# Performance work log

Measured on AMD Instinct MI355X. Metric: run time of the kernel, lower is better.

## Reference

```python
import jax, jax.numpy as jnp
import numpy as np

NUM_CLASSES = 19
TEMPERATURE = 0.2


def setup_inputs() -> dict:
    key = jax.random.key(0)
    k1, k2, k3 = jax.random.split(key, 3)
    fea = jax.random.normal(k1, (8, 256, 128, 128), dtype=jnp.float32)
    res = jax.random.normal(k2, (8, 19, 128, 128), dtype=jnp.float32)
    q = jax.random.normal(k3, (NUM_CLASSES, 256, 2975), dtype=jnp.float32)
    # buffers are L2-normalized along the feature (inner_planes) dim at init
    queues = q / jnp.maximum(jnp.linalg.norm(q, axis=1, keepdims=True), 1e-12)
    return {"fea": fea, "res": res, "queues": queues}


def _contrast_loss(fea, res, queues):
    # fea: [bs, C, H, W], res: [bs, K, H, W] logits, queues: [K, C, Q]
    bs, C = fea.shape[0], fea.shape[1]
    pred = jnp.argmax(res, axis=1).reshape(bs, -1)          # [bs, HW]
    ff = fea.reshape(bs, C, -1)                              # [bs, C, HW]

    # masked per-class region pooling across the whole batch (pred == val)
    onehot = (pred[:, :, None] == jnp.arange(NUM_CLASSES)[None, None, :]).astype(fea.dtype)  # [bs, HW, K]
    counts = onehot.sum(axis=(0, 1))                         # [K]
    sums = jnp.einsum('bcp,bpk->kc', ff, onehot)             # [K, C]
    keys = sums / jnp.maximum(counts, 1.0)[:, None]          # masked mean per class
    # F.normalize(keys, dim=1) with eps=1e-12
    keys = keys / jnp.maximum(jnp.linalg.norm(keys, axis=1, keepdims=True), 1e-12)

    # l_pos = q[:,None] * queue_c ; l_neg = q[:,None] * sum_{c'!=c} queue_c'
    qsum = queues.sum(axis=0)                                # [C, Q]
    l_pos = keys[:, :, None] * queues                        # [K, C, Q]
    l_neg = keys[:, :, None] * (qsum[None] - queues)         # [K, C, Q]
    logits = jnp.concatenate([l_pos, l_neg], axis=2) / TEMPERATURE  # [K, C, 2Q]

    # CrossEntropyLoss with labels all zero: mean over rows of (logsumexp - logit_0)
    lse = jax.nn.logsumexp(logits, axis=2)                   # [K, C]
    per_class = jnp.mean(lse - logits[:, :, 0], axis=1)      # [K]

    # original sums loss only over classes present in pred
    present = counts > 0
    return jnp.sum(jnp.where(present, per_class, jnp.zeros_like(per_class)))


def reference(fea, res, queues):
    contrast_loss = _contrast_loss(fea, res, queues)
    return (res, contrast_loss)
```

## Files before the change

kernel.cpp:

```cpp
#include <hip/hip_runtime.h>

#define HW 16384
#define BS 8
#define NC 256
#define K  19
#define Q  2975
#define INV_T 5.0f
#define NCHUNK 4
#define QC 744
#define NB1 512

__global__ void __launch_bounds__(256) k1_argmax(const float* __restrict__ res,
                                                 float* __restrict__ out,
                                                 unsigned char* __restrict__ pred,
                                                 int* __restrict__ histb,
                                                 float* __restrict__ sums) {
    __shared__ int hist[K];
    int t = threadIdx.x;
    if (t < K) hist[t] = 0;
    __syncthreads();
    int gp = blockIdx.x * 256 + t;
    int b  = gp >> 14;
    int p  = gp & (HW - 1);
    const float* rb = res + (size_t)b * K * HW + p;
    float*       ob = out + (size_t)b * K * HW + p;
    float best = rb[0];
    int   bk   = 0;
    __builtin_nontemporal_store(best, &ob[0]);
    #pragma unroll
    for (int k = 1; k < K; ++k) {
        float v = rb[(size_t)k * HW];
        __builtin_nontemporal_store(v, &ob[(size_t)k * HW]);
        if (v > best) { best = v; bk = k; }
    }
    pred[gp] = (unsigned char)bk;
    atomicAdd(&hist[bk], 1);
    if (blockIdx.x == 0) {
        for (int i = t; i < K * NC; i += 256) sums[i] = 0.f;
    }
    __syncthreads();
    if (t < K) histb[t * NB1 + blockIdx.x] = hist[t];
}

__global__ void __launch_bounds__(256) k2_pool(const float* __restrict__ fea,
                                               const unsigned char* __restrict__ pred,
                                               float* __restrict__ sums) {
    __shared__ float acc[K * 256];
    int t = threadIdx.x, lane = t & 63, w = t >> 6;
    int b = blockIdx.x >> 8;
    int c = blockIdx.x & 255;
    #pragma unroll
    for (int k = 0; k < K; ++k) acc[k * 256 + t] = 0.f;
    __syncthreads();
    const float4* f4 = (const float4*)(fea + (size_t)(b * NC + c) * HW);
    const uchar4* p4 = (const uchar4*)(pred + (size_t)b * HW);
    int c0 = t, c1 = (t + 64) & 255, c2 = (t + 128) & 255, c3 = (t + 192) & 255;
    #pragma unroll 2
    for (int i = t; i < HW / 4; i += 256) {
        float4 v  = f4[i];
        uchar4 kk = p4[i];
        int i0 = kk.x * 256 + c0, i1 = kk.y * 256 + c1;
        int i2 = kk.z * 256 + c2, i3 = kk.w * 256 + c3;
        float a0 = acc[i0], a1 = acc[i1], a2 = acc[i2], a3 = acc[i3];
        acc[i0] = a0 + v.x;
        acc[i1] = a1 + v.y;
        acc[i2] = a2 + v.z;
        acc[i3] = a3 + v.w;
    }
    __syncthreads();
    for (int k = w; k < K; k += 4) {
        float v = acc[k * 256 + lane]       + acc[k * 256 + lane + 64]
                + acc[k * 256 + lane + 128] + acc[k * 256 + lane + 192];
        #pragma unroll
        for (int off = 32; off > 0; off >>= 1) v += __shfl_xor(v, off, 64);
        if (lane == 0) atomicAdd(&sums[k * NC + c], v);
    }
}

__global__ void __launch_bounds__(256, 4) k4_lse(const float* __restrict__ queues,
                                                 const float* __restrict__ sums,
                                                 float* __restrict__ spart,
                                                 float* __restrict__ pos0) {
    int t = threadIdx.x;
    int c = blockIdx.x;
    int chunk = blockIdx.y;
    int lane = t & 63, wv = t >> 6;

    __shared__ float sc_sh[K];
    for (int k = wv; k < K; k += 4) {
        float ss = 0.f;
        #pragma unroll
        for (int j = 0; j < 4; ++j) {
            float v = sums[k * NC + j * 64 + lane];
            ss += v * v;
        }
        #pragma unroll
        for (int off = 32; off > 0; off >>= 1) ss += __shfl_xor(ss, off, 64);
        if (lane == 0) sc_sh[k] = INV_T / fmaxf(sqrtf(ss), 1e-12f);
    }
    __syncthreads();

    float key[K], s[K];
    #pragma unroll
    for (int k = 0; k < K; ++k) {
        key[k] = sums[k * NC + c] * sc_sh[k];
        s[k] = 0.f;
    }
    if (chunk == 0 && t < K)
        pos0[t * NC + c] = sums[t * NC + c] * sc_sh[t] * queues[(size_t)(t * NC + c) * Q];

    int q0 = chunk * QC;
    int qhi = min(Q, q0 + QC);
    for (int q = q0 + t; q < qhi; q += 256) {
        float qv[K];
        float qs = 0.f;
        #pragma unroll
        for (int k = 0; k < K; ++k) {
            qv[k] = queues[(size_t)(k * NC + c) * Q + q];
            qs += qv[k];
        }
        #pragma unroll
        for (int k = 0; k < K; ++k) {
            float a  = key[k] * qv[k];
            float bn = fmaf(key[k], qs, -a);
            s[k] += __expf(a) + __expf(bn);
        }
    }

    __shared__ float sw[K][4];
    #pragma unroll
    for (int k = 0; k < K; ++k) {
        float sk = s[k];
        #pragma unroll
        for (int off = 32; off > 0; off >>= 1) sk += __shfl_xor(sk, off, 64);
        if (lane == 0) sw[k][wv] = sk;
    }
    __syncthreads();
    if (t < K)
        spart[((size_t)t * NC + c) * NCHUNK + chunk] = sw[t][0] + sw[t][1] + sw[t][2] + sw[t][3];
}

__global__ void k5_final(const float* __restrict__ spart, const float* __restrict__ pos0,
                         const int* __restrict__ histb, float* __restrict__ loss) {
    __shared__ float cnt_sh[K];
    int t = threadIdx.x, lane = t & 63, w = t >> 6;
    for (int k = w; k < K; k += 4) {
        float cf = 0.f;
        #pragma unroll
        for (int j = 0; j < NB1 / 64; ++j)
            cf += (float)histb[k * NB1 + j * 64 + lane];
        #pragma unroll
        for (int off = 32; off > 0; off >>= 1) cf += __shfl_xor(cf, off, 64);
        if (lane == 0) cnt_sh[k] = cf;
    }
    __syncthreads();
    float acc = 0.f;
    #pragma unroll
    for (int k = 0; k < K; ++k) {
        float4 sp = ((const float4*)spart)[k * NC + t];
        float lse = logf(sp.x + sp.y + sp.z + sp.w);
        if (cnt_sh[k] > 0.5f) acc += lse - pos0[k * NC + t];
    }
    __shared__ float red[256];
    red[t] = acc;
    __syncthreads();
    for (int s = 128; s > 0; s >>= 1) {
        if (t < s) red[t] += red[t + s];
        __syncthreads();
    }
    if (t == 0) *loss = red[0] * (1.0f / 256.0f);
}

extern "C" void kernel_launch(void* const* d_in, const int* in_sizes, int n_in,
                              void* d_out, int out_size, void* d_ws, size_t ws_size,
                              hipStream_t stream) {
    const float* fea    = (const float*)d_in[0];
    const float* res    = (const float*)d_in[1];
    const float* queues = (const float*)d_in[2];

    float* out  = (float*)d_out;
    float* loss = out + (size_t)BS * K * HW;

    char* ws = (char*)d_ws;
    float*         sums   = (float*)(ws);
    int*           histb  = (int*)(ws + 19456);
    unsigned char* pred   = (unsigned char*)(ws + 58368);
    float*         spart  = (float*)(ws + 189440);
    float*         pos0   = (float*)(ws + 267264);

    hipLaunchKernelGGL(k1_argmax, dim3(NB1),        dim3(256), 0, stream, res, out, pred, histb, sums);
    hipLaunchKernelGGL(k2_pool,   dim3(BS * NC),    dim3(256), 0, stream, fea, pred, sums);
    hipLaunchKernelGGL(k4_lse,    dim3(NC, NCHUNK), dim3(256), 0, stream, queues, sums, spart, pos0);
    hipLaunchKernelGGL(k5_final,  dim3(1),          dim3(256), 0, stream, spart, pos0, histb, loss);
}
```

Baseline: 60.96 us.

## Fuse final loss reduction into LSE kernel with 1024-thread blocks and atomic accumulation

Removes the separate single-block final kernel by having each LSE block compute its per-channel loss contribution and atomically add it to the output scalar, which is zeroed in the argmax kernel. The LSE kernel now uses one 1024-thread block per channel instead of four 256-thread chunk blocks, so the partial-sum and pos0 workspace round trips go away. The pooling loop unroll is also raised. In exchange, each block does redundant histogram and norm preprocessing, the float atomic makes the summation order nondeterministic, and 1024-thread blocks holding 19-element register arrays may limit occupancy.

```diff
diff --git a/kernel.cpp b/kernel.cpp
--- a/kernel.cpp
+++ b/kernel.cpp
@@ -6,15 +6,14 @@
 #define K  19
 #define Q  2975
 #define INV_T 5.0f
-#define NCHUNK 4
-#define QC 744
 #define NB1 512
 
 __global__ void __launch_bounds__(256) k1_argmax(const float* __restrict__ res,
                                                  float* __restrict__ out,
                                                  unsigned char* __restrict__ pred,
                                                  int* __restrict__ histb,
-                                                 float* __restrict__ sums) {
+                                                 float* __restrict__ sums,
+                                                 float* __restrict__ loss) {
     __shared__ int hist[K];
     int t = threadIdx.x;
     if (t < K) hist[t] = 0;
@@ -37,6 +36,7 @@
     atomicAdd(&hist[bk], 1);
     if (blockIdx.x == 0) {
         for (int i = t; i < K * NC; i += 256) sums[i] = 0.f;
+        if (t == 0) *loss = 0.f;
     }
     __syncthreads();
     if (t < K) histb[t * NB1 + blockIdx.x] = hist[t];
@@ -55,7 +55,7 @@
     const float4* f4 = (const float4*)(fea + (size_t)(b * NC + c) * HW);
     const uchar4* p4 = (const uchar4*)(pred + (size_t)b * HW);
     int c0 = t, c1 = (t + 64) & 255, c2 = (t + 128) & 255, c3 = (t + 192) & 255;
-    #pragma unroll 2
+    #pragma unroll 4
     for (int i = t; i < HW / 4; i += 256) {
         float4 v  = f4[i];
         uchar4 kk = p4[i];
@@ -77,26 +77,34 @@
     }
 }
 
-__global__ void __launch_bounds__(256, 4) k4_lse(const float* __restrict__ queues,
-                                                 const float* __restrict__ sums,
-                                                 float* __restrict__ spart,
-                                                 float* __restrict__ pos0) {
+__global__ void __launch_bounds__(1024, 4) k4_lse(const float* __restrict__ queues,
+                                                  const float* __restrict__ sums,
+                                                  const int* __restrict__ histb,
+                                                  float* __restrict__ loss) {
     int t = threadIdx.x;
     int c = blockIdx.x;
-    int chunk = blockIdx.y;
     int lane = t & 63, wv = t >> 6;
 
-    __shared__ float sc_sh[K];
-    for (int k = wv; k < K; k += 4) {
-        float ss = 0.f;
+    __shared__ float sc_sh[K], cnt_sh[K];
+    for (int k = wv; k < K; k += 16) {
+        float ss = 0.f, cf = 0.f;
         #pragma unroll
         for (int j = 0; j < 4; ++j) {
             float v = sums[k * NC + j * 64 + lane];
             ss += v * v;
         }
         #pragma unroll
-        for (int off = 32; off > 0; off >>= 1) ss += __shfl_xor(ss, off, 64);
-        if (lane == 0) sc_sh[k] = INV_T / fmaxf(sqrtf(ss), 1e-12f);
+        for (int j = 0; j < NB1 / 64; ++j)
+            cf += (float)histb[k * NB1 + j * 64 + lane];
+        #pragma unroll
+        for (int off = 32; off > 0; off >>= 1) {
+            ss += __shfl_xor(ss, off, 64);
+            cf += __shfl_xor(cf, off, 64);
+        }
+        if (lane == 0) {
+            sc_sh[k]  = INV_T / fmaxf(sqrtf(ss), 1e-12f);
+            cnt_sh[k] = cf;
+        }
     }
     __syncthreads();
 
@@ -106,12 +114,8 @@
         key[k] = sums[k * NC + c] * sc_sh[k];
         s[k] = 0.f;
     }
-    if (chunk == 0 && t < K)
-        pos0[t * NC + c] = sums[t * NC + c] * sc_sh[t] * queues[(size_t)(t * NC + c) * Q];
 
-    int q0 = chunk * QC;
-    int qhi = min(Q, q0 + QC);
-    for (int q = q0 + t; q < qhi; q += 256) {
+    for (int q = t; q < Q; q += 1024) {
         float qv[K];
         float qs = 0.f;
         #pragma unroll
@@ -127,7 +131,7 @@
         }
     }
 
-    __shared__ float sw[K][4];
+    __shared__ float sw[K][16];
     #pragma unroll
     for (int k = 0; k < K; ++k) {
         float sk = s[k];
@@ -136,39 +140,23 @@
         if (lane == 0) sw[k][wv] = sk;
     }
     __syncthreads();
-    if (t < K)
-        spart[((size_t)t * NC + c) * NCHUNK + chunk] = sw[t][0] + sw[t][1] + sw[t][2] + sw[t][3];
-}
-
-__global__ void k5_final(const float* __restrict__ spart, const float* __restrict__ pos0,
-                         const int* __restrict__ histb, float* __restrict__ loss) {
-    __shared__ float cnt_sh[K];
-    int t = threadIdx.x, lane = t & 63, w = t >> 6;
-    for (int k = w; k < K; k += 4) {
-        float cf = 0.f;
+    __shared__ float red[32];
+    if (t < K) {
+        float S = 0.f;
         #pragma unroll
-        for (int j = 0; j < NB1 / 64; ++j)
-            cf += (float)histb[k * NB1 + j * 64 + lane];
-        #pragma unroll
-        for (int off = 32; off > 0; off >>= 1) cf += __shfl_xor(cf, off, 64);
-        if (lane == 0) cnt_sh[k] = cf;
+        for (int w2 = 0; w2 < 16; ++w2) S += sw[t][w2];
+        float lse   = logf(S);
+        float key_t = sums[t * NC + c] * sc_sh[t];
+        float pos0  = key_t * queues[(size_t)(t * NC + c) * Q];
+        red[t] = (cnt_sh[t] > 0.5f) ? (lse - pos0) : 0.f;
     }
     __syncthreads();
-    float acc = 0.f;
-    #pragma unroll
-    for (int k = 0; k < K; ++k) {
-        float4 sp = ((const float4*)spart)[k * NC + t];
-        float lse = logf(sp.x + sp.y + sp.z + sp.w);
-        if (cnt_sh[k] > 0.5f) acc += lse - pos0[k * NC + t];
+    if (t == 0) {
+        float acc = 0.f;
+        #pragma unroll
+        for (int k = 0; k < K; ++k) acc += red[k];
+        atomicAdd(loss, acc * (1.0f / 256.0f));
     }
-    __shared__ float red[256];
-    red[t] = acc;
-    __syncthreads();
-    for (int s = 128; s > 0; s >>= 1) {
-        if (t < s) red[t] += red[t + s];
-        __syncthreads();
-    }
-    if (t == 0) *loss = red[0] * (1.0f / 256.0f);
 }
 
 extern "C" void kernel_launch(void* const* d_in, const int* in_sizes, int n_in,
@@ -182,14 +170,11 @@
     float* loss = out + (size_t)BS * K * HW;
 
     char* ws = (char*)d_ws;
-    float*         sums   = (float*)(ws);
-    int*           histb  = (int*)(ws + 19456);
-    unsigned char* pred   = (unsigned char*)(ws + 58368);
-    float*         spart  = (float*)(ws + 189440);
-    float*         pos0   = (float*)(ws + 267264);
+    float*         sums  = (float*)(ws);
+    int*           histb = (int*)(ws + 19456);
+    unsigned char* pred  = (unsigned char*)(ws + 58368);
 
-    hipLaunchKernelGGL(k1_argmax, dim3(NB1),        dim3(256), 0, stream, res, out, pred, histb, sums);
-    hipLaunchKernelGGL(k2_pool,   dim3(BS * NC),    dim3(256), 0, stream, fea, pred, sums);
-    hipLaunchKernelGGL(k4_lse,    dim3(NC, NCHUNK), dim3(256), 0, stream, queues, sums, spart, pos0);
-    hipLaunchKernelGGL(k5_final,  dim3(1),          dim3(256), 0, stream, spart, pos0, histb, loss);
+    hipLaunchKernelGGL(k1_argmax, dim3(NB1),     dim3(256),  0, stream, res, out, pred, histb, sums, loss);
+    hipLaunchKernelGGL(k2_pool,   dim3(BS * NC), dim3(256),  0, stream, fea, pred, sums);
+    hipLaunchKernelGGL(k4_lse,    dim3(NC),      dim3(1024), 0, stream, queues, sums, histb, loss);
 }
```

Measured after the change: 50.79 us. 16.7% less time.
